# Kernel optimization log

Hardware: AMD Instinct MI355X
Metric: run time of the kernel (lower is better)

## Reference

```python
import jax, jax.numpy as jnp
import numpy as np

DIM = 1024
HIDDEN = 2048
NUM_EXPERTS = 8
TOP_K = 2


def setup_inputs() -> dict:
    key = jax.random.key(0)
    ks = jax.random.split(key, 6)
    scale = 0.02
    x = jax.random.normal(ks[0], (2, 4096, DIM), dtype=jnp.float32)
    # router: Linear(dim, num_experts, bias=False) -> weight [E, d]
    router_w = jax.random.normal(ks[1], (NUM_EXPERTS, DIM), dtype=jnp.float32) * scale
    # per-expert MLP: Linear(d, h) -> w1 [E, h, d], b1 [E, h]; Linear(h, d) -> w2 [E, d, h], b2 [E, d]
    w1 = jax.random.normal(ks[2], (NUM_EXPERTS, HIDDEN, DIM), dtype=jnp.float32) * scale
    b1 = jnp.zeros((NUM_EXPERTS, HIDDEN), dtype=jnp.float32)
    w2 = jax.random.normal(ks[3], (NUM_EXPERTS, DIM, HIDDEN), dtype=jnp.float32) * scale
    b2 = jnp.zeros((NUM_EXPERTS, DIM), dtype=jnp.float32)
    return {"x": x, "router_w": router_w, "w1": w1, "b1": b1, "w2": w2, "b2": b2}


def reference(x, router_w, w1, b1, w2, b2):
    b, s, d = x.shape
    xf = x.reshape(-1, d)                              # [T, d]
    logits = xf @ router_w.T                           # [T, E]
    all_probs = jax.nn.softmax(logits, axis=-1)
    topk_logits, topk_inds = jax.lax.top_k(logits, TOP_K)   # [T, K]
    topk_probs = jax.nn.softmax(topk_logits, axis=-1)
    E = router_w.shape[0]
    onehot = jax.nn.one_hot(topk_inds, E, dtype=xf.dtype)   # [T, K, E]
    # combine weights per (token, expert); zero where expert not selected
    gate = jnp.einsum('tke,tk->te', onehot, topk_probs)     # [T, E]
    # load-balancing auxiliary loss
    f_i = onehot.mean(axis=(0, 1))                          # [E]
    P_i = all_probs.mean(axis=0)                            # [E]
    aux_loss = E * jnp.sum(f_i * P_i)
    # dense per-expert MLP, weighted combine (dropout=0 / eval mode)
    out = jnp.zeros_like(xf)
    for e in range(E):  # fixed small loop over experts
        h = jax.nn.gelu(xf @ w1[e].T + b1[e], approximate=False)  # exact GELU (torch default)
        y = h @ w2[e].T + b2[e]
        out = out + gate[:, e:e + 1] * y
    return out.reshape(b, s, d), aux_loss
```

## Files before the change

### kernel.cpp

```cpp
#include <hip/hip_runtime.h>


#define TOKS 8192
#define DIMD 1024
#define HID  2048
#define NE   8

#define OFF_COUNTS   0
#define OFF_OFFSETS  64
#define OFF_CURSORS  128
#define OFF_TILEOFF  192
#define OFF_TOPKI    256
#define OFF_TOPKG    (OFF_TOPKI + TOKS*2*4)
#define OFF_BLKPS    (OFF_TOPKG + TOKS*2*4)
#define OFF_ATOK     (OFF_BLKPS + 2048*NE*4)
#define OFF_AGATE    (OFF_ATOK + TOKS*2*4)
#define OFF_PINV     (OFF_AGATE + TOKS*2*4)
#define OFF_XG       (1u << 20)
#define XG_ROWS      (TOKS*2 + 256)
#define OFF_W1B      (OFF_XG  + (size_t)XG_ROWS * DIMD * 2)
#define OFF_W2B      (OFF_W1B + (size_t)NE * HID * DIMD * 2)
#define OFF_H        (OFF_W2B + (size_t)NE * DIMD * HID * 2)
#define OFF_Y        (OFF_H   + (size_t)XG_ROWS * HID * 2)

typedef __bf16 bf16x8 __attribute__((ext_vector_type(8)));
typedef float  floatx4 __attribute__((ext_vector_type(4)));

__device__ __forceinline__ float bf2f(unsigned short u) {
    return __uint_as_float(((unsigned)u) << 16);
}
__device__ __forceinline__ unsigned short f2bf(float f) {
    unsigned u = __float_as_uint(f);
    unsigned r = (u + 0x7FFFu + ((u >> 16) & 1u)) >> 16;
    return (unsigned short)r;
}

#define GLOBAL_AS(p) ((const __attribute__((address_space(1))) unsigned int*)(p))
#define LDS_AS(p)    ((__attribute__((address_space(3))) unsigned int*)(p))

__device__ __forceinline__ int xcd_remap(int bid, int nwg) {
    int xcd = bid & 7, pos = bid >> 3;
    int q = nwg >> 3, r = nwg & 7;
    int start = (xcd < r) ? xcd * (q + 1) : r * (q + 1) + (xcd - r) * q;
    return start + pos;
}

__global__ void convert_w_kernel(const float4* __restrict__ w1,
                                 ushort4* __restrict__ w1b, int n1,
                                 const float4* __restrict__ w2,
                                 ushort4* __restrict__ w2b, int n2) {
    int i = blockIdx.x * blockDim.x + threadIdx.x;
    int stride = gridDim.x * blockDim.x;
    int ntot = n1 + n2;
    for (; i < ntot; i += stride) {
        float4 v; ushort4 o;
        if (i < n1) v = w1[i]; else v = w2[i - n1];
        o.x = f2bf(v.x); o.y = f2bf(v.y); o.z = f2bf(v.z); o.w = f2bf(v.w);
        if (i < n1) w1b[i] = o; else w2b[i - n1] = o;
    }
}

__global__ __launch_bounds__(256) void router_kernel(
    const float* __restrict__ x, const float* __restrict__ rw,
    int* __restrict__ topki, float* __restrict__ topkg,
    float* __restrict__ blkps)
{
    int wave = threadIdx.x >> 6;
    int lane = threadIdx.x & 63;
    int t = blockIdx.x * 4 + wave;
    const float* xt = x + (size_t)t * DIMD;

    float acc[NE];
#pragma unroll
    for (int e = 0; e < NE; e++) acc[e] = 0.f;
    for (int i = 0; i < DIMD / 64; i++) {
        float xv = xt[lane + 64 * i];
#pragma unroll
        for (int e = 0; e < NE; e++) acc[e] += xv * rw[e * DIMD + lane + 64 * i];
    }
#pragma unroll
    for (int off = 32; off > 0; off >>= 1) {
#pragma unroll
        for (int e = 0; e < NE; e++) acc[e] += __shfl_down(acc[e], off);
    }

    __shared__ float ps[4][NE];
    if (lane == 0) {
        float m = acc[0];
#pragma unroll
        for (int e = 1; e < NE; e++) m = fmaxf(m, acc[e]);
        float ex[NE], s = 0.f;
#pragma unroll
        for (int e = 0; e < NE; e++) { ex[e] = expf(acc[e] - m); s += ex[e]; }
        float inv = 1.f / s;
#pragma unroll
        for (int e = 0; e < NE; e++) ps[wave][e] = ex[e] * inv;

        int i0 = 0; float l0 = acc[0];
#pragma unroll
        for (int e = 1; e < NE; e++) if (acc[e] > l0) { l0 = acc[e]; i0 = e; }
        int i1 = -1; float l1 = -3.4e38f;
#pragma unroll
        for (int e = 0; e < NE; e++) if (e != i0 && acc[e] > l1) { l1 = acc[e]; i1 = e; }
        float e1 = expf(l1 - l0);
        float g0 = 1.f / (1.f + e1);
        float g1 = e1 * g0;
        topki[t * 2 + 0] = i0; topki[t * 2 + 1] = i1;
        topkg[t * 2 + 0] = g0; topkg[t * 2 + 1] = g1;
    }
    __syncthreads();
    if (threadIdx.x < NE) {
        float s = ps[0][threadIdx.x] + ps[1][threadIdx.x] + ps[2][threadIdx.x] + ps[3][threadIdx.x];
        blkps[blockIdx.x * NE + threadIdx.x] = s;
    }
}

__global__ __launch_bounds__(256) void finalize_kernel(
    const int* __restrict__ topki, const float* __restrict__ blkps,
    int* __restrict__ counts, int* __restrict__ offsets, int* __restrict__ cursors,
    int* __restrict__ tileoff, float* __restrict__ aux_out)
{
    __shared__ float psum[NE];
    __shared__ int cnt[NE];
    int tid = threadIdx.x;
    if (tid < NE) { psum[tid] = 0.f; cnt[tid] = 0; }
    __syncthreads();

    float lp[NE]; int lc[NE];
#pragma unroll
    for (int e = 0; e < NE; e++) { lp[e] = 0.f; lc[e] = 0; }
    const float4* bp4 = (const float4*)blkps;
    for (int i = tid; i < 2048 * NE / 4; i += 256) {
        float4 v = bp4[i];
        int eb = (4 * i) & 7;
        lp[eb + 0] += v.x; lp[eb + 1] += v.y; lp[eb + 2] += v.z; lp[eb + 3] += v.w;
    }
    const int4* ti4 = (const int4*)topki;
    for (int i = tid; i < TOKS * 2 / 4; i += 256) {
        int4 v = ti4[i];
        lc[v.x]++; lc[v.y]++; lc[v.z]++; lc[v.w]++;
    }
#pragma unroll
    for (int e = 0; e < NE; e++) { atomicAdd(&psum[e], lp[e]); atomicAdd(&cnt[e], lc[e]); }
    __syncthreads();

    if (tid == 0) {
        int off = 0, to = 0;
        for (int e = 0; e < NE; e++) {
            counts[e] = cnt[e];
            offsets[e] = off; cursors[e] = off;
            tileoff[e] = to;
            off += cnt[e];
            to += (cnt[e] + 255) >> 8;
        }
        offsets[NE] = off; tileoff[NE] = to;
        float aux = 0.f;
        for (int e = 0; e < NE; e++)
            aux += ((float)cnt[e] / (float)(TOKS * 2)) * (psum[e] / (float)TOKS);
        aux_out[0] = (float)NE * aux;
    }
}

__global__ __launch_bounds__(64) void fill_kernel(
    const int* __restrict__ topki, const float* __restrict__ topkg,
    int* __restrict__ cursors, int* __restrict__ atok, float* __restrict__ agate,
    int* __restrict__ posinv)
{
    int lane = threadIdx.x;
    int t = blockIdx.x * 64 + lane;
    unsigned long long below = (lane == 63) ? 0x7FFFFFFFFFFFFFFFull
                                            : ((1ull << lane) - 1ull);
#pragma unroll
    for (int k = 0; k < 2; k++) {
        int e = topki[t * 2 + k];
        float g = topkg[t * 2 + k];
        for (int ee = 0; ee < NE; ee++) {
            bool pred = (e == ee);
            unsigned long long mask = __ballot(pred ? 1 : 0);
            if (mask) {
                int leader = __ffsll((unsigned long long)mask) - 1;
                int base = 0;
                if (lane == leader) base = atomicAdd(&cursors[ee], (int)__popcll(mask));
                base = __shfl(base, leader);
                if (pred) {
                    int pos = base + (int)__popcll(mask & below);
                    atok[pos] = t;
                    agate[pos] = g;
                    posinv[t * 2 + k] = pos;
                }
            }
        }
    }
}

__global__ __launch_bounds__(256) void gather_x_kernel(
    const float* __restrict__ x, const int* __restrict__ atok,
    ushort* __restrict__ Xg)
{
    int r = blockIdx.x;
    int tid = threadIdx.x;
    int tok = atok[r];
    float4 v = ((const float4*)(x + (size_t)tok * DIMD))[tid];
    ushort4 o;
    o.x = f2bf(v.x); o.y = f2bf(v.y); o.z = f2bf(v.z); o.w = f2bf(v.w);
    ((ushort4*)(Xg + (size_t)r * DIMD))[tid] = o;
}

template<int LD, int NT>
__device__ __forceinline__ void gemm_fat(
    const ushort* __restrict__ gApanel, const ushort* __restrict__ gBpanel,
    ushort (&lds)[2][64][512], floatx4 (&acc)[8][4],
    int lane, int wave, int wr, int wc, int l15, int quad)
{
    auto stage_tile = [&](int bsel, int u) {
#pragma unroll
        for (int t = 0; t < 2; t++) {
            int s = wave * 2 + t;
            const ushort* a0 = gApanel + (size_t)(s * 16 + l15) * LD + u * 64 + quad * 8;
            __builtin_amdgcn_global_load_lds(GLOBAL_AS(a0),
                LDS_AS(&lds[bsel][s * 2 + 0][0]), 16, 0, 0);
            __builtin_amdgcn_global_load_lds(GLOBAL_AS(a0 + 32),
                LDS_AS(&lds[bsel][s * 2 + 1][0]), 16, 0, 0);
            const ushort* b0 = gBpanel + (size_t)(s * 16 + l15) * LD + u * 64 + quad * 8;
            __builtin_amdgcn_global_load_lds(GLOBAL_AS(b0),
                LDS_AS(&lds[bsel][32 + s * 2 + 0][0]), 16, 0, 0);
            __builtin_amdgcn_global_load_lds(GLOBAL_AS(b0 + 32),
                LDS_AS(&lds[bsel][32 + s * 2 + 1][0]), 16, 0, 0);
        }
    };

#pragma unroll
    for (int i = 0; i < 8; i++)
#pragma unroll
        for (int j = 0; j < 4; j++) acc[i][j] = (floatx4){0.f, 0.f, 0.f, 0.f};

    stage_tile(0, 0);
    stage_tile(1, 1);
    asm volatile("s_waitcnt vmcnt(8)");
    __builtin_amdgcn_s_barrier();
    __builtin_amdgcn_sched_barrier(0);

    for (int u = 0; u < NT; u++) {
        const bf16x8* C = (const bf16x8*)&lds[u & 1][0][0];
        bf16x8 af[8][2], bfr[4][2];
#pragma unroll
        for (int mi = 0; mi < 8; mi++) {
            af[mi][0] = C[((wr * 8 + mi) * 2 + 0) * 64 + lane];
            af[mi][1] = C[((wr * 8 + mi) * 2 + 1) * 64 + lane];
        }
#pragma unroll
        for (int nj = 0; nj < 4; nj++) {
            bfr[nj][0] = C[(32 + (wc * 4 + nj) * 2 + 0) * 64 + lane];
            bfr[nj][1] = C[(32 + (wc * 4 + nj) * 2 + 1) * 64 + lane];
        }
        __builtin_amdgcn_sched_barrier(0);
        asm volatile("s_waitcnt lgkmcnt(0)");
        __builtin_amdgcn_s_barrier();
        __builtin_amdgcn_sched_barrier(0);
        if (u + 2 < NT) stage_tile(u & 1, u + 2);
        __builtin_amdgcn_s_setprio(1);
#pragma unroll
        for (int mi = 0; mi < 8; mi++)
#pragma unroll
            for (int nj = 0; nj < 4; nj++) {
                acc[mi][nj] = __builtin_amdgcn_mfma_f32_16x16x32_bf16(
                    af[mi][0], bfr[nj][0], acc[mi][nj], 0, 0, 0);
                acc[mi][nj] = __builtin_amdgcn_mfma_f32_16x16x32_bf16(
                    af[mi][1], bfr[nj][1], acc[mi][nj], 0, 0, 0);
            }
        __builtin_amdgcn_s_setprio(0);
        if (u + 1 < NT) {
            if (u + 2 < NT) asm volatile("s_waitcnt vmcnt(8)");
            else            asm volatile("s_waitcnt vmcnt(0)");
        }
        __builtin_amdgcn_s_barrier();
        __builtin_amdgcn_sched_barrier(0);
    }
}

__global__ __launch_bounds__(512, 2) void phase1_kernel(
    const ushort* __restrict__ Xg, const ushort* __restrict__ w1b,
    const float* __restrict__ b1,
    const int* __restrict__ counts, const int* __restrict__ offsets,
    const int* __restrict__ tileoff, unsigned short* __restrict__ Hbuf)
{
    const int NCOLT = HID / 256;
    int total = tileoff[NE] * NCOLT;
    int idx = xcd_remap((int)blockIdx.x, (int)gridDim.x);
    if (idx >= total) return;
    int ct = idx & (NCOLT - 1);
    int rowt = idx / NCOLT;
    int e = 0;
    while (rowt >= tileoff[e + 1]) e++;
    int row0 = (rowt - tileoff[e]) * 256;
    int cnt = counts[e];
    int base = offsets[e];
    int colbase = ct * 256;

    __shared__ ushort lds[2][64][512];

    int tid = threadIdx.x;
    int lane = tid & 63;
    int wave = tid >> 6;
    int wr = wave >> 2, wc = wave & 3;
    int l15 = lane & 15, quad = lane >> 4;

    const ushort* gApanel = Xg + (size_t)(base + row0) * DIMD;
    const ushort* gBpanel = w1b + (size_t)e * HID * DIMD + (size_t)colbase * DIMD;

    floatx4 acc[8][4];
    gemm_fat<DIMD, DIMD / 64>(gApanel, gBpanel, lds, acc, lane, wave, wr, wc, l15, quad);

    float b1v[4];
#pragma unroll
    for (int j = 0; j < 4; j++)
        b1v[j] = b1[e * HID + colbase + 64 * wc + 16 * j + l15];
#pragma unroll
    for (int i = 0; i < 8; i++) {
#pragma unroll
        for (int rr = 0; rr < 4; rr++) {
            int pr = row0 + 128 * wr + 16 * i + quad * 4 + rr;
            if (pr < cnt) {
                size_t hrow = (size_t)(base + pr) * HID;
#pragma unroll
                for (int j = 0; j < 4; j++) {
                    int col = colbase + 64 * wc + 16 * j + l15;
                    float v = acc[i][j][rr] + b1v[j];
                    v = 0.5f * v * (1.f + erff(v * 0.70710678118654752f));
                    Hbuf[hrow + col] = f2bf(v);
                }
            }
        }
    }
}

__global__ __launch_bounds__(512, 2) void phase2_kernel(
    const ushort* __restrict__ Hbuf, const ushort* __restrict__ w2b,
    const int* __restrict__ counts, const int* __restrict__ offsets,
    const int* __restrict__ tileoff, ushort* __restrict__ Y)
{
    const int NCOLT = DIMD / 256;
    int total = tileoff[NE] * NCOLT;
    int idx = xcd_remap((int)blockIdx.x, (int)gridDim.x);
    if (idx >= total) return;
    int ct = idx & (NCOLT - 1);
    int rowt = idx / NCOLT;
    int e = 0;
    while (rowt >= tileoff[e + 1]) e++;
    int row0 = (rowt - tileoff[e]) * 256;
    int cnt = counts[e];
    int base = offsets[e];
    int colbase = ct * 256;

    __shared__ ushort lds[2][64][512];

    int tid = threadIdx.x;
    int lane = tid & 63;
    int wave = tid >> 6;
    int wr = wave >> 2, wc = wave & 3;
    int l15 = lane & 15, quad = lane >> 4;

    const ushort* gApanel = Hbuf + (size_t)(base + row0) * HID;
    const ushort* gBpanel = w2b + (size_t)e * DIMD * HID + (size_t)colbase * HID;

    floatx4 acc[8][4];
    gemm_fat<HID, HID / 64>(gApanel, gBpanel, lds, acc, lane, wave, wr, wc, l15, quad);

#pragma unroll
    for (int i = 0; i < 8; i++) {
#pragma unroll
        for (int rr = 0; rr < 4; rr++) {
            int pr = row0 + 128 * wr + 16 * i + quad * 4 + rr;
            if (pr < cnt) {
                size_t yrow = (size_t)(base + pr) * DIMD;
#pragma unroll
                for (int j = 0; j < 4; j++) {
                    int col = colbase + 64 * wc + 16 * j + l15;
                    Y[yrow + col] = f2bf(acc[i][j][rr]);
                }
            }
        }
    }
}

__global__ __launch_bounds__(256) void combine_kernel(
    const ushort* __restrict__ Y, const float* __restrict__ b2,
    const int* __restrict__ topki, const float* __restrict__ topkg,
    const int* __restrict__ posinv, float* __restrict__ out)
{
    int wave = threadIdx.x >> 6;
    int lane = threadIdx.x & 63;
    int t = blockIdx.x * 4 + wave;
    int e0 = topki[t * 2 + 0], e1 = topki[t * 2 + 1];
    float g0 = topkg[t * 2 + 0], g1 = topkg[t * 2 + 1];
    int p0 = posinv[t * 2 + 0], p1 = posinv[t * 2 + 1];

    const ushort4* y0 = (const ushort4*)(Y + (size_t)p0 * DIMD);
    const ushort4* y1 = (const ushort4*)(Y + (size_t)p1 * DIMD);
    const float4* b20 = (const float4*)(b2 + (size_t)e0 * DIMD);
    const float4* b21 = (const float4*)(b2 + (size_t)e1 * DIMD);
    float4* o4 = (float4*)(out + (size_t)t * DIMD);

#pragma unroll
    for (int c = 0; c < DIMD / 4 / 64; c++) {
        int i = lane + 64 * c;
        ushort4 a = y0[i], b = y1[i];
        float4 ba = b20[i], bb = b21[i];
        float4 r;
        r.x = g0 * (bf2f(a.x) + ba.x) + g1 * (bf2f(b.x) + bb.x);
        r.y = g0 * (bf2f(a.y) + ba.y) + g1 * (bf2f(b.y) + bb.y);
        r.z = g0 * (bf2f(a.z) + ba.z) + g1 * (bf2f(b.z) + bb.z);
        r.w = g0 * (bf2f(a.w) + ba.w) + g1 * (bf2f(b.w) + bb.w);
        o4[i] = r;
    }
}

extern "C" void kernel_launch(void* const* d_in, const int* in_sizes, int n_in,
                              void* d_out, int out_size, void* d_ws, size_t ws_size,
                              hipStream_t stream) {
    const float* x  = (const float*)d_in[0];
    const float* rw = (const float*)d_in[1];
    const float* w1 = (const float*)d_in[2];
    const float* b1 = (const float*)d_in[3];
    const float* w2 = (const float*)d_in[4];
    const float* b2 = (const float*)d_in[5];
    float* out = (float*)d_out;

    char* ws = (char*)d_ws;
    int*   counts  = (int*)(ws + OFF_COUNTS);
    int*   offsets = (int*)(ws + OFF_OFFSETS);
    int*   cursors = (int*)(ws + OFF_CURSORS);
    int*   tileoff = (int*)(ws + OFF_TILEOFF);
    int*   topki   = (int*)(ws + OFF_TOPKI);
    float* topkg   = (float*)(ws + OFF_TOPKG);
    float* blkps   = (float*)(ws + OFF_BLKPS);
    int*   atok    = (int*)(ws + OFF_ATOK);
    float* agate   = (float*)(ws + OFF_AGATE);
    int*   posinv  = (int*)(ws + OFF_PINV);
    ushort* Xg     = (ushort*)(ws + OFF_XG);
    ushort* w1b    = (ushort*)(ws + OFF_W1B);
    ushort* w2b    = (ushort*)(ws + OFF_W2B);
    ushort* Hbuf   = (ushort*)(ws + OFF_H);
    ushort* Y      = (ushort*)(ws + OFF_Y);

    convert_w_kernel<<<8192, 256, 0, stream>>>(
        (const float4*)w1, (ushort4*)w1b, NE * HID * DIMD / 4,
        (const float4*)w2, (ushort4*)w2b, NE * DIMD * HID / 4);

    router_kernel<<<TOKS / 4, 256, 0, stream>>>(x, rw, topki, topkg, blkps);
    finalize_kernel<<<1, 256, 0, stream>>>(topki, blkps, counts, offsets, cursors,
                                           tileoff, out + (size_t)TOKS * DIMD);
    fill_kernel<<<TOKS / 64, 64, 0, stream>>>(topki, topkg, cursors, atok, agate,
                                              posinv);
    gather_x_kernel<<<TOKS * 2, 256, 0, stream>>>(x, atok, Xg);

    phase1_kernel<<<71 * (HID / 256), 512, 0, stream>>>(
        Xg, w1b, b1, counts, offsets, tileoff, Hbuf);
    phase2_kernel<<<71 * (DIMD / 256), 512, 0, stream>>>(
        Hbuf, w2b, counts, offsets, tileoff, Y);
    combine_kernel<<<TOKS / 4, 256, 0, stream>>>(Y, b2, topki, topkg, posinv, out);
}
```

Before: 593.1 us.

## Shrink GEMM tiles to 256x128 with single-stage prefetch and scatter-style gather

Replaces the 256x256 tile GEMM, which used explicit waitcnt and a two-ahead prefetch, with a 256x128 tile over a K-step of 32. It uses a simpler one-ahead double buffer with __syncthreads and a smaller LDS footprint, so four blocks can fit per CU. Per-wave accumulators drop from 8x4 to 4x4 fragments, which raises occupancy and doubles the grid. The cost is less data reuse per tile and more barriers per unit of K. The gather kernel now reads each token row once and writes it to both of its expert slots through posinv, instead of reading x twice.

```diff
diff --git a/kernel.cpp b/kernel.cpp
--- a/kernel.cpp
+++ b/kernel.cpp
@@ -194,97 +194,71 @@
 }
 
 __global__ __launch_bounds__(256) void gather_x_kernel(
-    const float* __restrict__ x, const int* __restrict__ atok,
+    const float* __restrict__ x, const int* __restrict__ posinv,
     ushort* __restrict__ Xg)
 {
-    int r = blockIdx.x;
+    int t = blockIdx.x;
     int tid = threadIdx.x;
-    int tok = atok[r];
-    float4 v = ((const float4*)(x + (size_t)tok * DIMD))[tid];
+    float4 v = ((const float4*)(x + (size_t)t * DIMD))[tid];
     ushort4 o;
     o.x = f2bf(v.x); o.y = f2bf(v.y); o.z = f2bf(v.z); o.w = f2bf(v.w);
-    ((ushort4*)(Xg + (size_t)r * DIMD))[tid] = o;
+    int p0 = posinv[t * 2 + 0], p1 = posinv[t * 2 + 1];
+    ((ushort4*)(Xg + (size_t)p0 * DIMD))[tid] = o;
+    ((ushort4*)(Xg + (size_t)p1 * DIMD))[tid] = o;
 }
 
 template<int LD, int NT>
-__device__ __forceinline__ void gemm_fat(
+__device__ __forceinline__ void gemm_tlp(
     const ushort* __restrict__ gApanel, const ushort* __restrict__ gBpanel,
-    ushort (&lds)[2][64][512], floatx4 (&acc)[8][4],
+    ushort (&lds)[2][24][512], floatx4 (&acc)[4][4],
     int lane, int wave, int wr, int wc, int l15, int quad)
 {
-    auto stage_tile = [&](int bsel, int u) {
+    auto stage = [&](int bsel, int u) {
 #pragma unroll
         for (int t = 0; t < 2; t++) {
             int s = wave * 2 + t;
-            const ushort* a0 = gApanel + (size_t)(s * 16 + l15) * LD + u * 64 + quad * 8;
+            const ushort* a0 = gApanel + (size_t)(s * 16 + l15) * LD + u * 32 + quad * 8;
             __builtin_amdgcn_global_load_lds(GLOBAL_AS(a0),
-                LDS_AS(&lds[bsel][s * 2 + 0][0]), 16, 0, 0);
-            __builtin_amdgcn_global_load_lds(GLOBAL_AS(a0 + 32),
-                LDS_AS(&lds[bsel][s * 2 + 1][0]), 16, 0, 0);
-            const ushort* b0 = gBpanel + (size_t)(s * 16 + l15) * LD + u * 64 + quad * 8;
-            __builtin_amdgcn_global_load_lds(GLOBAL_AS(b0),
-                LDS_AS(&lds[bsel][32 + s * 2 + 0][0]), 16, 0, 0);
-            __builtin_amdgcn_global_load_lds(GLOBAL_AS(b0 + 32),
-                LDS_AS(&lds[bsel][32 + s * 2 + 1][0]), 16, 0, 0);
+                LDS_AS(&lds[bsel][s][0]), 16, 0, 0);
         }
+        const ushort* b0 = gBpanel + (size_t)(wave * 16 + l15) * LD + u * 32 + quad * 8;
+        __builtin_amdgcn_global_load_lds(GLOBAL_AS(b0),
+            LDS_AS(&lds[bsel][16 + wave][0]), 16, 0, 0);
     };
 
 #pragma unroll
-    for (int i = 0; i < 8; i++)
+    for (int i = 0; i < 4; i++)
 #pragma unroll
         for (int j = 0; j < 4; j++) acc[i][j] = (floatx4){0.f, 0.f, 0.f, 0.f};
 
-    stage_tile(0, 0);
-    stage_tile(1, 1);
-    asm volatile("s_waitcnt vmcnt(8)");
-    __builtin_amdgcn_s_barrier();
-    __builtin_amdgcn_sched_barrier(0);
+    stage(0, 0);
+    __syncthreads();
 
     for (int u = 0; u < NT; u++) {
+        if (u + 1 < NT) stage((u + 1) & 1, u + 1);
         const bf16x8* C = (const bf16x8*)&lds[u & 1][0][0];
-        bf16x8 af[8][2], bfr[4][2];
-#pragma unroll
-        for (int mi = 0; mi < 8; mi++) {
-            af[mi][0] = C[((wr * 8 + mi) * 2 + 0) * 64 + lane];
-            af[mi][1] = C[((wr * 8 + mi) * 2 + 1) * 64 + lane];
-        }
-#pragma unroll
-        for (int nj = 0; nj < 4; nj++) {
-            bfr[nj][0] = C[(32 + (wc * 4 + nj) * 2 + 0) * 64 + lane];
-            bfr[nj][1] = C[(32 + (wc * 4 + nj) * 2 + 1) * 64 + lane];
-        }
-        __builtin_amdgcn_sched_barrier(0);
-        asm volatile("s_waitcnt lgkmcnt(0)");
-        __builtin_amdgcn_s_barrier();
-        __builtin_amdgcn_sched_barrier(0);
-        if (u + 2 < NT) stage_tile(u & 1, u + 2);
-        __builtin_amdgcn_s_setprio(1);
-#pragma unroll
-        for (int mi = 0; mi < 8; mi++)
-#pragma unroll
-            for (int nj = 0; nj < 4; nj++) {
+        bf16x8 a[4], b[4];
+#pragma unroll
+        for (int mi = 0; mi < 4; mi++) a[mi] = C[(wr * 4 + mi) * 64 + lane];
+#pragma unroll
+        for (int nj = 0; nj < 4; nj++) b[nj] = C[(16 + wc * 4 + nj) * 64 + lane];
+#pragma unroll
+        for (int mi = 0; mi < 4; mi++)
+#pragma unroll
+            for (int nj = 0; nj < 4; nj++)
                 acc[mi][nj] = __builtin_amdgcn_mfma_f32_16x16x32_bf16(
-                    af[mi][0], bfr[nj][0], acc[mi][nj], 0, 0, 0);
-                acc[mi][nj] = __builtin_amdgcn_mfma_f32_16x16x32_bf16(
-                    af[mi][1], bfr[nj][1], acc[mi][nj], 0, 0, 0);
-            }
-        __builtin_amdgcn_s_setprio(0);
-        if (u + 1 < NT) {
-            if (u + 2 < NT) asm volatile("s_waitcnt vmcnt(8)");
-            else            asm volatile("s_waitcnt vmcnt(0)");
-        }
-        __builtin_amdgcn_s_barrier();
-        __builtin_amdgcn_sched_barrier(0);
-    }
-}
-
-__global__ __launch_bounds__(512, 2) void phase1_kernel(
+                    a[mi], b[nj], acc[mi][nj], 0, 0, 0);
+        __syncthreads();
+    }
+}
+
+__global__ __launch_bounds__(512, 4) void phase1_kernel(
     const ushort* __restrict__ Xg, const ushort* __restrict__ w1b,
     const float* __restrict__ b1,
     const int* __restrict__ counts, const int* __restrict__ offsets,
     const int* __restrict__ tileoff, unsigned short* __restrict__ Hbuf)
 {
-    const int NCOLT = HID / 256;
+    const int NCOLT = HID / 128;
     int total = tileoff[NE] * NCOLT;
     int idx = xcd_remap((int)blockIdx.x, (int)gridDim.x);
     if (idx >= total) return;
@@ -295,31 +269,31 @@
     int row0 = (rowt - tileoff[e]) * 256;
     int cnt = counts[e];
     int base = offsets[e];
-    int colbase = ct * 256;
-
-    __shared__ ushort lds[2][64][512];
+    int colbase = ct * 128;
+
+    __shared__ ushort lds[2][24][512];
 
     int tid = threadIdx.x;
     int lane = tid & 63;
     int wave = tid >> 6;
-    int wr = wave >> 2, wc = wave & 3;
+    int wr = wave >> 1, wc = wave & 1;
     int l15 = lane & 15, quad = lane >> 4;
 
     const ushort* gApanel = Xg + (size_t)(base + row0) * DIMD;
     const ushort* gBpanel = w1b + (size_t)e * HID * DIMD + (size_t)colbase * DIMD;
 
-    floatx4 acc[8][4];
-    gemm_fat<DIMD, DIMD / 64>(gApanel, gBpanel, lds, acc, lane, wave, wr, wc, l15, quad);
+    floatx4 acc[4][4];
+    gemm_tlp<DIMD, DIMD / 32>(gApanel, gBpanel, lds, acc, lane, wave, wr, wc, l15, quad);
 
     float b1v[4];
 #pragma unroll
     for (int j = 0; j < 4; j++)
         b1v[j] = b1[e * HID + colbase + 64 * wc + 16 * j + l15];
 #pragma unroll
-    for (int i = 0; i < 8; i++) {
+    for (int i = 0; i < 4; i++) {
 #pragma unroll
         for (int rr = 0; rr < 4; rr++) {
-            int pr = row0 + 128 * wr + 16 * i + quad * 4 + rr;
+            int pr = row0 + 64 * wr + 16 * i + quad * 4 + rr;
             if (pr < cnt) {
                 size_t hrow = (size_t)(base + pr) * HID;
 #pragma unroll
@@ -334,12 +308,12 @@
     }
 }
 
-__global__ __launch_bounds__(512, 2) void phase2_kernel(
+__global__ __launch_bounds__(512, 4) void phase2_kernel(
     const ushort* __restrict__ Hbuf, const ushort* __restrict__ w2b,
     const int* __restrict__ counts, const int* __restrict__ offsets,
     const int* __restrict__ tileoff, ushort* __restrict__ Y)
 {
-    const int NCOLT = DIMD / 256;
+    const int NCOLT = DIMD / 128;
     int total = tileoff[NE] * NCOLT;
     int idx = xcd_remap((int)blockIdx.x, (int)gridDim.x);
     if (idx >= total) return;
@@ -350,27 +324,27 @@
     int row0 = (rowt - tileoff[e]) * 256;
     int cnt = counts[e];
     int base = offsets[e];
-    int colbase = ct * 256;
-
-    __shared__ ushort lds[2][64][512];
+    int colbase = ct * 128;
+
+    __shared__ ushort lds[2][24][512];
 
     int tid = threadIdx.x;
     int lane = tid & 63;
     int wave = tid >> 6;
-    int wr = wave >> 2, wc = wave & 3;
+    int wr = wave >> 1, wc = wave & 1;
     int l15 = lane & 15, quad = lane >> 4;
 
     const ushort* gApanel = Hbuf + (size_t)(base + row0) * HID;
     const ushort* gBpanel = w2b + (size_t)e * DIMD * HID + (size_t)colbase * HID;
 
-    floatx4 acc[8][4];
-    gemm_fat<HID, HID / 64>(gApanel, gBpanel, lds, acc, lane, wave, wr, wc, l15, quad);
-
-#pragma unroll
-    for (int i = 0; i < 8; i++) {
+    floatx4 acc[4][4];
+    gemm_tlp<HID, HID / 32>(gApanel, gBpanel, lds, acc, lane, wave, wr, wc, l15, quad);
+
+#pragma unroll
+    for (int i = 0; i < 4; i++) {
 #pragma unroll
         for (int rr = 0; rr < 4; rr++) {
-            int pr = row0 + 128 * wr + 16 * i + quad * 4 + rr;
+            int pr = row0 + 64 * wr + 16 * i + quad * 4 + rr;
             if (pr < cnt) {
                 size_t yrow = (size_t)(base + pr) * DIMD;
 #pragma unroll
@@ -452,11 +426,11 @@
                                            tileoff, out + (size_t)TOKS * DIMD);
     fill_kernel<<<TOKS / 64, 64, 0, stream>>>(topki, topkg, cursors, atok, agate,
                                               posinv);
-    gather_x_kernel<<<TOKS * 2, 256, 0, stream>>>(x, atok, Xg);
-
-    phase1_kernel<<<71 * (HID / 256), 512, 0, stream>>>(
+    gather_x_kernel<<<TOKS, 256, 0, stream>>>(x, posinv, Xg);
+
+    phase1_kernel<<<71 * (HID / 128), 512, 0, stream>>>(
         Xg, w1b, b1, counts, offsets, tileoff, Hbuf);
-    phase2_kernel<<<71 * (DIMD / 256), 512, 0, stream>>>(
+    phase2_kernel<<<71 * (DIMD / 128), 512, 0, stream>>>(
         Hbuf, w2b, counts, offsets, tileoff, Y);
     combine_kernel<<<TOKS / 4, 256, 0, stream>>>(Y, b2, topki, topkg, posinv, out);
 }
```

After: 592.8 us. No clear change (-0.0%).
